# Kernel optimization log

Hardware: AMD Instinct MI355X
Metric: run time of the kernel (lower is better)

## Reference

```python
import jax, jax.numpy as jnp
import numpy as np

B, C, W, H = 4, 256, 64, 64
DK = C // 8  # query/key channels


def setup_inputs() -> dict:
    key = jax.random.key(0)
    ks = jax.random.split(key, 7)
    x = jax.random.normal(ks[0], (B, C, W, H), dtype=jnp.float32)
    # conv1x1 weights stored as [out_ch, in_ch]
    Wq = jax.random.normal(ks[1], (DK, C), dtype=jnp.float32) / np.sqrt(C)
    bq = jnp.zeros((DK,), dtype=jnp.float32)
    Wk = jax.random.normal(ks[2], (DK, C), dtype=jnp.float32) / np.sqrt(C)
    bk = jnp.zeros((DK,), dtype=jnp.float32)
    Wv = jax.random.normal(ks[3], (C, C), dtype=jnp.float32) / np.sqrt(C)
    bv = jnp.zeros((C,), dtype=jnp.float32)
    gamma = jnp.zeros((1,), dtype=jnp.float32)
    return {"x": x, "Wq": Wq, "bq": bq, "Wk": Wk, "bk": bk,
            "Wv": Wv, "bv": bv, "gamma": gamma}


def reference(x, Wq, bq, Wk, bk, Wv, bv, gamma):
    b, c, w, h = x.shape
    n = w * h
    xf = x.reshape(b, c, n)                     # [B, C, N]
    # conv1x1 == channel matmul
    q = jnp.einsum('dc,bcn->bnd', Wq, xf) + bq  # [B, N, DK]
    k = jnp.einsum('dc,bcn->bdn', Wk, xf) + bk[None, :, None]  # [B, DK, N]
    energy = jnp.einsum('bnd,bdm->bnm', q, k)   # [B, N, N]
    attention = jax.nn.softmax(energy, axis=-1)
    v = jnp.einsum('dc,bcn->bdn', Wv, xf) + bv[None, :, None]  # [B, C, N]
    out = jnp.einsum('bdm,bnm->bdn', v, attention)              # [B, C, N]
    out = out.reshape(b, c, w, h)
    out = gamma * out + x
    return out, attention
```

## Files before the change

### kernel.cpp

```cpp
#include <hip/hip_runtime.h>
#include <hip/hip_bf16.h>

typedef __attribute__((ext_vector_type(8))) short bf16x8;
typedef __attribute__((ext_vector_type(4))) float f32x4;
typedef __attribute__((ext_vector_type(4))) unsigned int u32x4;
typedef __attribute__((ext_vector_type(2))) unsigned int u32x2;

#define B_SZ 4
#define C_SZ 256
#define N_SZ 4096
#define DK_SZ 32

#define WQB_OFF 0
#define WKB_OFF 8192
#define WVB_OFF 16384
#define QB_OFF  81920
#define KB_OFF  606208
#define VB_OFF  1130496

__device__ __forceinline__ short f2bf(float f) {
    union { float f; unsigned int u; } v; v.f = f;
    unsigned int r = v.u + 0x7fffu + ((v.u >> 16) & 1u);
    return (short)(r >> 16);
}

__device__ __forceinline__ unsigned int cvt_pk_bf16(float lo, float hi) {
    unsigned int r;
    asm volatile("v_cvt_pk_bf16_f32 %0, %1, %2" : "=v"(r) : "v"(lo), "v"(hi));
    return r;
}

__device__ __forceinline__ f32x4 mfma16(bf16x8 a, bf16x8 b, f32x4 c) {
    return __builtin_amdgcn_mfma_f32_16x16x32_bf16(a, b, c, 0, 0, 0);
}

__device__ __forceinline__ void gload_lds16(const void* g, void* l) {
    __builtin_amdgcn_global_load_lds((const __attribute__((address_space(1))) unsigned int*)g,
                                     (__attribute__((address_space(3))) unsigned int*)l, 16, 0, 0);
}

__device__ __forceinline__ void remap_block(int i, int& b, int& n0) {
    b = (i & 7) >> 1;
    n0 = (((i >> 3) << 1) | (i & 1)) * 64;
}

__global__ __launch_bounds__(256) void k_convw(const float* __restrict__ Wq,
                                               const float* __restrict__ Wk,
                                               const float* __restrict__ Wv,
                                               short* __restrict__ ws) {
    int i = blockIdx.x * 256 + threadIdx.x;
    if (i < 8192) {
        ws[WQB_OFF + i] = f2bf(Wq[i]);
        ws[WKB_OFF + i] = f2bf(Wk[i]);
    }
    ws[WVB_OFF + i] = f2bf(Wv[i]);
}

__global__ __launch_bounds__(256) void k_prep(const float* __restrict__ x,
                                              const float* __restrict__ bq,
                                              const float* __restrict__ bk,
                                              const float* __restrict__ bv,
                                              short* __restrict__ ws) {
    __shared__ short xsT[64][264];
    __shared__ short vt_s[64][258];

    int b, n0;
    remap_block(blockIdx.x, b, n0);
    const int t = threadIdx.x;
    const float* xb = x + (size_t)b * C_SZ * N_SZ;

    {
        int c0 = t >> 4, n4 = (t & 15) * 4;
#pragma unroll
        for (int i = 0; i < 16; i++) {
            int c = c0 + 16 * i;
            float4 v = *(const float4*)(xb + (size_t)c * N_SZ + n0 + n4);
            xsT[n4 + 0][c] = f2bf(v.x);
            xsT[n4 + 1][c] = f2bf(v.y);
            xsT[n4 + 2][c] = f2bf(v.z);
            xsT[n4 + 3][c] = f2bf(v.w);
        }
    }
    __syncthreads();

    const int w = t >> 6, l = t & 63;
    const int lr = l & 15, lk = l >> 4;

    bf16x8 af[8];
#pragma unroll
    for (int kk = 0; kk < 8; kk++)
        af[kk] = *(const bf16x8*)(&xsT[w * 16 + lr][kk * 32 + lk * 8]);

#pragma unroll
    for (int qk = 0; qk < 2; qk++) {
        const short* wb = ws + (qk ? WKB_OFF : WQB_OFF);
        const float* bias = qk ? bk : bq;
        short* outp = ws + (qk ? KB_OFF : QB_OFF) + (size_t)b * N_SZ * DK_SZ;
#pragma unroll
        for (int cf = 0; cf < 2; cf++) {
            f32x4 acc = {0.f, 0.f, 0.f, 0.f};
#pragma unroll
            for (int kk = 0; kk < 8; kk++) {
                bf16x8 bfr = *(const bf16x8*)(wb + (cf * 16 + lr) * 256 + kk * 32 + lk * 8);
                acc = mfma16(af[kk], bfr, acc);
            }
            float bias_v = bias[cf * 16 + lr];
#pragma unroll
            for (int r = 0; r < 4; r++) {
                int row = w * 16 + lk * 4 + r;
                outp[(size_t)(n0 + row) * DK_SZ + cf * 16 + lr] = f2bf(acc[r] + bias_v);
            }
        }
    }

#pragma unroll
    for (int cf = 0; cf < 16; cf++) {
        f32x4 acc = {0.f, 0.f, 0.f, 0.f};
#pragma unroll
        for (int kk = 0; kk < 8; kk++) {
            bf16x8 bfr = *(const bf16x8*)(ws + WVB_OFF + (cf * 16 + lr) * 256 + kk * 32 + lk * 8);
            acc = mfma16(af[kk], bfr, acc);
        }
        float bias_v = bv[cf * 16 + lr];
#pragma unroll
        for (int r = 0; r < 4; r++) {
            vt_s[w * 16 + lk * 4 + r][cf * 16 + lr] = f2bf(acc[r] + bias_v);
        }
    }
    __syncthreads();
    {
        short* vb = ws + VB_OFF + (size_t)b * C_SZ * N_SZ;
        int nn = t & 63;
#pragma unroll
        for (int i = 0; i < 64; i++) {
            int c = (t >> 6) + 4 * i;
            vb[(size_t)c * N_SZ + n0 + nn] = vt_s[nn][c];
        }
    }
}

__global__ __launch_bounds__(512, 1) void k_attn(const short* __restrict__ ws,
                                                 const float* __restrict__ x,
                                                 const float* __restrict__ gamma_p,
                                                 float* __restrict__ out) {
    __shared__ short v_lds[3][16384];
    __shared__ short k_lds[3][2304];
    __shared__ float rsum_s[2][64];

    int b, n0;
    remap_block(blockIdx.x, b, n0);
    const int t = threadIdx.x, w = t >> 6, l = t & 63;
    const int rg = w & 3, ch = w >> 2;
    const int lr = l & 15, lk = l >> 4;

    const short* qb = ws + QB_OFF + (size_t)b * N_SZ * DK_SZ;
    const short* kb = ws + KB_OFF + (size_t)b * N_SZ * DK_SZ;
    const short* vb = ws + VB_OFF + (size_t)b * C_SZ * N_SZ;
    const char* kbb = (const char*)kb;

    bf16x8 qf = *(const bf16x8*)(qb + (size_t)(n0 + rg * 16 + lr) * DK_SZ + lk * 8);

    float rs = 0.f;
    for (int mt = 0; mt < 32; mt++) {
        int mb = ch * 2048 + mt * 64;
        bf16x8 kfa = *(const bf16x8*)(kb + (size_t)(mb + lr) * DK_SZ + lk * 8);
        bf16x8 kfb = *(const bf16x8*)(kb + (size_t)(mb + 16 + lr) * DK_SZ + lk * 8);
        bf16x8 kfc = *(const bf16x8*)(kb + (size_t)(mb + 32 + lr) * DK_SZ + lk * 8);
        bf16x8 kfd = *(const bf16x8*)(kb + (size_t)(mb + 48 + lr) * DK_SZ + lk * 8);
        f32x4 s0 = mfma16(kfa, qf, (f32x4){0.f, 0.f, 0.f, 0.f});
        f32x4 s1 = mfma16(kfb, qf, (f32x4){0.f, 0.f, 0.f, 0.f});
        f32x4 s2 = mfma16(kfc, qf, (f32x4){0.f, 0.f, 0.f, 0.f});
        f32x4 s3 = mfma16(kfd, qf, (f32x4){0.f, 0.f, 0.f, 0.f});
#pragma unroll
        for (int r = 0; r < 4; r++)
            rs += __expf(s0[r]) + __expf(s1[r]) + __expf(s2[r]) + __expf(s3[r]);
    }
    rs += __shfl_xor(rs, 16);
    rs += __shfl_xor(rs, 32);
    if (l < 16) rsum_s[ch][rg * 16 + l] = rs;
    __syncthreads();
    const float invp = 1.f / (rsum_s[0][rg * 16 + lr] + rsum_s[1][rg * 16 + lr]);

    float* attn_row = out + (size_t)B_SZ * C_SZ * N_SZ + (size_t)b * N_SZ * N_SZ
                      + (size_t)(n0 + rg * 16 + lr) * N_SZ;
    f32x4 O[16];
#pragma unroll
    for (int cb = 0; cb < 16; cb++) O[cb] = (f32x4){0.f, 0.f, 0.f, 0.f};

    const bool odd = lk & 1;
    const bool swp = ((lk >> 1) ^ (lk & 1)) & 1;
    const bool hi  = lk >> 1;
    const int krow = ch * 32 + lr;
    const int kswz = ((lk ^ ((lr >> 1) & 3)) << 4);
    const int voff = lr * 128 + ((((ch << 2) + lk) ^ (lr & 7)) << 4);

    bf16x8 kf0, kf1, pf, pfN;

#define STAGE(tt, buf)                                                              \
    {                                                                               \
        const int krw = w * 8 + (l >> 2);                                           \
        const int ksl = (l & 3) ^ ((l >> 3) & 3);                                   \
        gload_lds16(kbb + (size_t)(tt) * 4096 + krw * 64 + ksl * 16,                \
                    (void*)&k_lds[buf][w * 256]);                                   \
        const int mb = (tt) * 64;                                                   \
        _Pragma("unroll")                                                           \
        for (int i = 0; i < 4; i++) {                                               \
            int c = w * 32 + i * 8 + (l >> 3);                                      \
            int j = l & 7;                                                          \
            const short* gp = vb + (size_t)c * N_SZ + mb + ((j ^ (c & 7)) << 3);    \
            gload_lds16(gp, (void*)&v_lds[buf][(w * 32 + i * 8) * 64]);             \
        }                                                                           \
    }

#define KREAD(tt)                                                                   \
    {                                                                               \
        const char* kl = (const char*)&k_lds[(tt) % 3][0];                          \
        kf0 = *(const bf16x8*)(kl + krow * 64 + kswz);                              \
        kf1 = *(const bf16x8*)(kl + krow * 64 + 1024 + kswz);                       \
    }

#define SCOMP_BODY(tt)                                                              \
    {                                                                               \
        f32x4 s0 = mfma16(kf0, qf, (f32x4){0.f, 0.f, 0.f, 0.f});                    \
        f32x4 s1 = mfma16(kf1, qf, (f32x4){0.f, 0.f, 0.f, 0.f});                    \
        f32x4 ev0, ev1;                                                             \
        ev0[0] = __expf(s0[0]) * invp; ev0[1] = __expf(s0[1]) * invp;               \
        ev0[2] = __expf(s0[2]) * invp; ev0[3] = __expf(s0[3]) * invp;               \
        ev1[0] = __expf(s1[0]) * invp; ev1[1] = __expf(s1[1]) * invp;               \
        ev1[2] = __expf(s1[2]) * invp; ev1[3] = __expf(s1[3]) * invp;               \
        const int mbase = (tt) * 64 + ch * 32 + 4 * lk;                             \
        __builtin_nontemporal_store(ev0, (f32x4*)(attn_row + mbase));               \
        __builtin_nontemporal_store(ev1, (f32x4*)(attn_row + mbase + 16));          \
        unsigned pkA0 = cvt_pk_bf16(ev0[0], ev0[1]);                                \
        unsigned pkA1 = cvt_pk_bf16(ev0[2], ev0[3]);                                \
        unsigned pkB0 = cvt_pk_bf16(ev1[0], ev1[1]);                                \
        unsigned pkB1 = cvt_pk_bf16(ev1[2], ev1[3]);                                \
        unsigned sw0 = odd ? pkA0 : pkB0;                                           \
        unsigned sw1 = odd ? pkA1 : pkB1;                                           \
        unsigned R0 = __shfl_xor(sw0, 16);                                          \
        unsigned R1 = __shfl_xor(sw1, 16);                                          \
        unsigned Kp0 = odd ? pkB0 : pkA0;                                           \
        unsigned Kp1 = odd ? pkB1 : pkA1;                                           \
        unsigned x0 = __shfl_xor(Kp0, 48); Kp0 = swp ? x0 : Kp0;                    \
        unsigned x1 = __shfl_xor(Kp1, 48); Kp1 = swp ? x1 : Kp1;                    \
        unsigned x2 = __shfl_xor(R0, 48);  R0  = swp ? x2 : R0;                     \
        unsigned x3 = __shfl_xor(R1, 48);  R1  = swp ? x3 : R1;                     \
        u32x4 pw;                                                                   \
        pw[0] = hi ? R0 : Kp0; pw[1] = hi ? R1 : Kp1;                               \
        pw[2] = hi ? Kp0 : R0; pw[3] = hi ? Kp1 : R1;                               \
        pfN = __builtin_bit_cast(bf16x8, pw);                                       \
    }

    STAGE(0, 0);
    STAGE(1, 1);
    __builtin_amdgcn_sched_barrier(0);
    asm volatile("s_waitcnt vmcnt(5)" ::: "memory");
    __builtin_amdgcn_sched_barrier(0);
    __builtin_amdgcn_s_barrier();
    KREAD(0);
    SCOMP_BODY(0);
    pf = pfN;

    for (int mt = 0; mt < 64; mt++) {
        asm volatile("s_waitcnt vmcnt(2) lgkmcnt(0)" ::: "memory");
        __builtin_amdgcn_sched_barrier(0);
        __builtin_amdgcn_s_barrier();
        __builtin_amdgcn_sched_barrier(0);
        const char* vbase = (const char*)&v_lds[mt % 3][0];
        if (mt < 63) KREAD(mt + 1);
        bf16x8 A1[8];
#pragma unroll
        for (int cb = 0; cb < 8; cb++)
            A1[cb] = *(const bf16x8*)(vbase + cb * 2048 + voff);
        if (mt < 62) STAGE(mt + 2, (mt + 2) % 3);
        __builtin_amdgcn_sched_barrier(0);
        if (mt < 63) SCOMP_BODY(mt + 1);
        __builtin_amdgcn_sched_barrier(0);
        bf16x8 A2[8];
#pragma unroll
        for (int cb = 0; cb < 8; cb++)
            A2[cb] = *(const bf16x8*)(vbase + (cb + 8) * 2048 + voff);
#pragma unroll
        for (int cb = 0; cb < 8; cb++) O[cb] = mfma16(A1[cb], pf, O[cb]);
#pragma unroll
        for (int cb = 0; cb < 8; cb++) O[cb + 8] = mfma16(A2[cb], pf, O[cb + 8]);
        pf = pfN;
    }
#undef STAGE
#undef KREAD
#undef SCOMP_BODY

    __syncthreads();
    float* o_red = (float*)&v_lds[0][0];
    const int RSTRIDE = 4360;
    if (ch == 1) {
#pragma unroll
        for (int cb = 0; cb < 16; cb++)
#pragma unroll
            for (int r = 0; r < 4; r++)
                o_red[rg * RSTRIDE + (cb * 16 + 4 * lk + r) * 17 + lr] = O[cb][r];
    }
    __syncthreads();
    if (ch == 0) {
#pragma unroll
        for (int cb = 0; cb < 16; cb++)
#pragma unroll
            for (int r = 0; r < 4; r++) {
                int idx = rg * RSTRIDE + (cb * 16 + 4 * lk + r) * 17 + lr;
                o_red[idx] += O[cb][r];
            }
    }
    __syncthreads();
    {
        const float g = gamma_p[0];
        const float* xb = x + (size_t)b * C_SZ * N_SZ;
        float* ob = out + (size_t)b * C_SZ * N_SZ;
        int nn = t & 63;
        int c0 = t >> 6;
        int rbase = (nn >> 4) * RSTRIDE + (nn & 15);
#pragma unroll
        for (int i = 0; i < 32; i++) {
            int c = c0 + 8 * i;
            size_t idx = (size_t)c * N_SZ + n0 + nn;
            ob[idx] = g * o_red[rbase + c * 17] + xb[idx];
        }
    }
}

extern "C" void kernel_launch(void* const* d_in, const int* in_sizes, int n_in,
                              void* d_out, int out_size, void* d_ws, size_t ws_size,
                              hipStream_t stream) {
    const float* x     = (const float*)d_in[0];
    const float* Wq    = (const float*)d_in[1];
    const float* bq    = (const float*)d_in[2];
    const float* Wk    = (const float*)d_in[3];
    const float* bk    = (const float*)d_in[4];
    const float* Wv    = (const float*)d_in[5];
    const float* bv    = (const float*)d_in[6];
    const float* gamma = (const float*)d_in[7];
    short* ws = (short*)d_ws;
    float* out = (float*)d_out;

    hipLaunchKernelGGL(k_convw, dim3(256), dim3(256), 0, stream, Wq, Wk, Wv, ws);
    hipLaunchKernelGGL(k_prep, dim3(256), dim3(256), 0, stream, x, bq, bk, bv, ws);
    hipLaunchKernelGGL(k_attn, dim3(256), dim3(512), 0, stream, ws, x, gamma, out);
}
```

Before: 137.4 us.

## Share softmax probabilities via LDS and retile PV matmul as 4x4 fragment blocks

```diff
diff --git a/kernel.cpp b/kernel.cpp
--- a/kernel.cpp
+++ b/kernel.cpp
@@ -145,6 +145,7 @@
                                                  float* __restrict__ out) {
     __shared__ short v_lds[3][16384];
     __shared__ short k_lds[3][2304];
+    __shared__ short p_lds[2][64][72];
     __shared__ float rsum_s[2][64];
 
     int b, n0;
@@ -183,18 +184,18 @@
 
     float* attn_row = out + (size_t)B_SZ * C_SZ * N_SZ + (size_t)b * N_SZ * N_SZ
                       + (size_t)(n0 + rg * 16 + lr) * N_SZ;
-    f32x4 O[16];
-#pragma unroll
-    for (int cb = 0; cb < 16; cb++) O[cb] = (f32x4){0.f, 0.f, 0.f, 0.f};
-
-    const bool odd = lk & 1;
-    const bool swp = ((lk >> 1) ^ (lk & 1)) & 1;
-    const bool hi  = lk >> 1;
+    f32x4 O[4][4];
+#pragma unroll
+    for (int cf = 0; cf < 4; cf++)
+#pragma unroll
+        for (int rgi = 0; rgi < 4; rgi++) O[cf][rgi] = (f32x4){0.f, 0.f, 0.f, 0.f};
+
     const int krow = ch * 32 + lr;
     const int kswz = ((lk ^ ((lr >> 1) & 3)) << 4);
-    const int voff = lr * 128 + ((((ch << 2) + lk) ^ (lr & 7)) << 4);
-
-    bf16x8 kf0, kf1, pf, pfN;
+    const int aoff = rg * 8192 + lr * 128 + ((((ch << 2) + lk) ^ (lr & 7)) << 4);
+    const int boff = lr * 144 + ch * 64 + lk * 16;
+
+    bf16x8 kf0, kf1;
 
 #define STAGE(tt, buf)                                                              \
     {                                                                               \
@@ -219,7 +220,7 @@
         kf1 = *(const bf16x8*)(kl + krow * 64 + 1024 + kswz);                       \
     }
 
-#define SCOMP_BODY(tt)                                                              \
+#define SCOMP_BODY(tt, pb)                                                          \
     {                                                                               \
         f32x4 s0 = mfma16(kf0, qf, (f32x4){0.f, 0.f, 0.f, 0.f});                    \
         f32x4 s1 = mfma16(kf1, qf, (f32x4){0.f, 0.f, 0.f, 0.f});                    \
@@ -231,24 +232,11 @@
         const int mbase = (tt) * 64 + ch * 32 + 4 * lk;                             \
         __builtin_nontemporal_store(ev0, (f32x4*)(attn_row + mbase));               \
         __builtin_nontemporal_store(ev1, (f32x4*)(attn_row + mbase + 16));          \
-        unsigned pkA0 = cvt_pk_bf16(ev0[0], ev0[1]);                                \
-        unsigned pkA1 = cvt_pk_bf16(ev0[2], ev0[3]);                                \
-        unsigned pkB0 = cvt_pk_bf16(ev1[0], ev1[1]);                                \
-        unsigned pkB1 = cvt_pk_bf16(ev1[2], ev1[3]);                                \
-        unsigned sw0 = odd ? pkA0 : pkB0;                                           \
-        unsigned sw1 = odd ? pkA1 : pkB1;                                           \
-        unsigned R0 = __shfl_xor(sw0, 16);                                          \
-        unsigned R1 = __shfl_xor(sw1, 16);                                          \
-        unsigned Kp0 = odd ? pkB0 : pkA0;                                           \
-        unsigned Kp1 = odd ? pkB1 : pkA1;                                           \
-        unsigned x0 = __shfl_xor(Kp0, 48); Kp0 = swp ? x0 : Kp0;                    \
-        unsigned x1 = __shfl_xor(Kp1, 48); Kp1 = swp ? x1 : Kp1;                    \
-        unsigned x2 = __shfl_xor(R0, 48);  R0  = swp ? x2 : R0;                     \
-        unsigned x3 = __shfl_xor(R1, 48);  R1  = swp ? x3 : R1;                     \
-        u32x4 pw;                                                                   \
-        pw[0] = hi ? R0 : Kp0; pw[1] = hi ? R1 : Kp1;                               \
-        pw[2] = hi ? Kp0 : R0; pw[3] = hi ? Kp1 : R1;                               \
-        pfN = __builtin_bit_cast(bf16x8, pw);                                       \
+        u32x2 pk0, pk1;                                                             \
+        pk0[0] = cvt_pk_bf16(ev0[0], ev0[1]); pk0[1] = cvt_pk_bf16(ev0[2], ev0[3]); \
+        pk1[0] = cvt_pk_bf16(ev1[0], ev1[1]); pk1[1] = cvt_pk_bf16(ev1[2], ev1[3]); \
+        *(u32x2*)(&p_lds[pb][rg * 16 + lr][ch * 32 + lk * 4]) = pk0;                \
+        *(u32x2*)(&p_lds[pb][rg * 16 + lr][ch * 32 + 16 + lk * 4]) = pk1;           \
     }
 
     STAGE(0, 0);
@@ -258,33 +246,33 @@
     __builtin_amdgcn_sched_barrier(0);
     __builtin_amdgcn_s_barrier();
     KREAD(0);
-    SCOMP_BODY(0);
-    pf = pfN;
+    SCOMP_BODY(0, 0);
 
     for (int mt = 0; mt < 64; mt++) {
         asm volatile("s_waitcnt vmcnt(2) lgkmcnt(0)" ::: "memory");
         __builtin_amdgcn_sched_barrier(0);
         __builtin_amdgcn_s_barrier();
         __builtin_amdgcn_sched_barrier(0);
-        const char* vbase = (const char*)&v_lds[mt % 3][0];
+        const int cur = mt & 1;
         if (mt < 63) KREAD(mt + 1);
-        bf16x8 A1[8];
-#pragma unroll
-        for (int cb = 0; cb < 8; cb++)
-            A1[cb] = *(const bf16x8*)(vbase + cb * 2048 + voff);
         if (mt < 62) STAGE(mt + 2, (mt + 2) % 3);
         __builtin_amdgcn_sched_barrier(0);
-        if (mt < 63) SCOMP_BODY(mt + 1);
+        if (mt < 63) SCOMP_BODY(mt + 1, cur ^ 1);
         __builtin_amdgcn_sched_barrier(0);
-        bf16x8 A2[8];
-#pragma unroll
-        for (int cb = 0; cb < 8; cb++)
-            A2[cb] = *(const bf16x8*)(vbase + (cb + 8) * 2048 + voff);
-#pragma unroll
-        for (int cb = 0; cb < 8; cb++) O[cb] = mfma16(A1[cb], pf, O[cb]);
-#pragma unroll
-        for (int cb = 0; cb < 8; cb++) O[cb + 8] = mfma16(A2[cb], pf, O[cb + 8]);
-        pf = pfN;
+        const char* vbase = (const char*)&v_lds[mt % 3][0];
+        const char* pbase = (const char*)&p_lds[cur][0][0];
+        bf16x8 Afr[4], Bfr[4];
+#pragma unroll
+        for (int cf = 0; cf < 4; cf++)
+            Afr[cf] = *(const bf16x8*)(vbase + cf * 2048 + aoff);
+#pragma unroll
+        for (int rgi = 0; rgi < 4; rgi++)
+            Bfr[rgi] = *(const bf16x8*)(pbase + rgi * 2304 + boff);
+#pragma unroll
+        for (int cf = 0; cf < 4; cf++)
+#pragma unroll
+            for (int rgi = 0; rgi < 4; rgi++)
+                O[cf][rgi] = mfma16(Afr[cf], Bfr[rgi], O[cf][rgi]);
     }
 #undef STAGE
 #undef KREAD
@@ -295,20 +283,24 @@
     const int RSTRIDE = 4360;
     if (ch == 1) {
 #pragma unroll
-        for (int cb = 0; cb < 16; cb++)
-#pragma unroll
-            for (int r = 0; r < 4; r++)
-                o_red[rg * RSTRIDE + (cb * 16 + 4 * lk + r) * 17 + lr] = O[cb][r];
+        for (int cf = 0; cf < 4; cf++)
+#pragma unroll
+            for (int rgi = 0; rgi < 4; rgi++)
+#pragma unroll
+                for (int r = 0; r < 4; r++)
+                    o_red[rgi * RSTRIDE + (rg * 64 + cf * 16 + 4 * lk + r) * 17 + lr] = O[cf][rgi][r];
     }
     __syncthreads();
     if (ch == 0) {
 #pragma unroll
-        for (int cb = 0; cb < 16; cb++)
-#pragma unroll
-            for (int r = 0; r < 4; r++) {
-                int idx = rg * RSTRIDE + (cb * 16 + 4 * lk + r) * 17 + lr;
-                o_red[idx] += O[cb][r];
-            }
+        for (int cf = 0; cf < 4; cf++)
+#pragma unroll
+            for (int rgi = 0; rgi < 4; rgi++)
+#pragma unroll
+                for (int r = 0; r < 4; r++) {
+                    int idx = rgi * RSTRIDE + (rg * 64 + cf * 16 + 4 * lk + r) * 17 + lr;
+                    o_red[idx] += O[cf][rgi][r];
+                }
     }
     __syncthreads();
     {
```

New measurement: 137.3 us. About the same (-0.1%).
